# Performance work log

Measured on AMD Instinct MI355X. Metric: run time of the kernel, lower is better.

Reference implementation:

```python
import jax, jax.numpy as jnp
import numpy as np

NUM_FEATURES = 27

def _tril_indices(F):
    idx = []
    for i in range(F):
        for j in range(i):
            idx.append(i * F + j)
    return np.asarray(idx, dtype=np.int32)

TRIL_IDX = _tril_indices(NUM_FEATURES)  # [F*(F-1)/2] = [351]


def setup_inputs() -> dict:
    key = jax.random.key(0)
    k1, k2 = jax.random.split(key)
    B, F, D = 65536, NUM_FEATURES, 128
    features = jax.random.normal(k1, (B, F, D), dtype=jnp.float32)
    bottom_mlp_out = jax.random.normal(k2, (B, D), dtype=jnp.float32)
    return {"features": features, "bottom_mlp_out": bottom_mlp_out}


def reference(features, bottom_mlp_out):
    # features: [B, F, D]
    B = features.shape[0]
    F = features.shape[1]
    # batched Gram matrix: [B, F, F]
    interactions = jnp.einsum('bfd,bgd->bfg', features, features)
    interactions = interactions.reshape(B, F * F)
    # strict lower-triangular pairs: [B, F*(F-1)/2]
    x = interactions[:, TRIL_IDX]
    # concat bottom MLP output in front: [B, D + F*(F-1)/2]
    return jnp.concatenate([bottom_mlp_out, x], axis=1)
```

## Files before the change

### kernel.cpp

```cpp
#include <hip/hip_runtime.h>
#include <stdint.h>

#define NF 27
#define ND 128
#define OUTW 479
#define WAVES 4

typedef float f32x4 __attribute__((ext_vector_type(4)));
typedef short s16x8 __attribute__((ext_vector_type(8)));

__device__ __forceinline__ unsigned short f2bf(float x) {
    union { float f; uint32_t u; } c; c.f = x;
    uint32_t u = c.u;
    u += 0x7fffu + ((u >> 16) & 1u);
    return (unsigned short)(u >> 16);
}

__device__ __forceinline__ s16x8 pack8(float4 a, float4 b) {
    s16x8 r;
    r[0] = (short)f2bf(a.x); r[1] = (short)f2bf(a.y);
    r[2] = (short)f2bf(a.z); r[3] = (short)f2bf(a.w);
    r[4] = (short)f2bf(b.x); r[5] = (short)f2bf(b.y);
    r[6] = (short)f2bf(b.z); r[7] = (short)f2bf(b.w);
    return r;
}

__global__ __launch_bounds__(256) void dot_interact_kernel(
    const float* __restrict__ feat,
    const float* __restrict__ bottom,
    float* __restrict__ out, int B)
{
    const int tid  = threadIdx.x;
    const int lane = tid & 63;
    const int b    = blockIdx.x * WAVES + (tid >> 6);
    if (b >= B) return;

    const int rsel = lane & 15;
    const int kg   = (lane >> 4) * 8;
    const int row1 = (rsel + 16 < NF) ? rsel + 16 : NF - 1;
    const float* fb = feat + (size_t)b * (NF * ND);
    const float* p0 = fb + rsel * ND + kg;
    const float* p1 = fb + row1 * ND + kg;

    f32x4 acc00 = {0.f,0.f,0.f,0.f};
    f32x4 acc10 = {0.f,0.f,0.f,0.f};
    f32x4 acc11 = {0.f,0.f,0.f,0.f};
    #pragma unroll
    for (int ks = 0; ks < 4; ++ks) {
        float4 a0 = *(const float4*)(p0 + ks * 32);
        float4 a1 = *(const float4*)(p0 + ks * 32 + 4);
        float4 b0 = *(const float4*)(p1 + ks * 32);
        float4 b1 = *(const float4*)(p1 + ks * 32 + 4);
        s16x8 fr0 = pack8(a0, a1);
        s16x8 fr1 = pack8(b0, b1);
        acc00 = __builtin_amdgcn_mfma_f32_16x16x32_bf16(fr0, fr0, acc00, 0, 0, 0);
        acc10 = __builtin_amdgcn_mfma_f32_16x16x32_bf16(fr1, fr0, acc10, 0, 0, 0);
        acc11 = __builtin_amdgcn_mfma_f32_16x16x32_bf16(fr1, fr1, acc11, 0, 0, 0);
    }

    float* ob = out + (size_t)b * OUTW;

    const float* bb = bottom + (size_t)b * ND;
    ob[lane]      = bb[lane];
    ob[lane + 64] = bb[lane + 64];

    const int jj = lane & 15;
    const int r0 = (lane >> 4) * 4;
    #pragma unroll
    for (int e = 0; e < 4; ++e) {
        int i0 = r0 + e;
        if (jj < i0) ob[128 + (i0 * (i0 - 1)) / 2 + jj] = acc00[e];
        int i1 = i0 + 16;
        if (i1 < NF) {
            ob[128 + (i1 * (i1 - 1)) / 2 + jj] = acc10[e];
            int j1 = jj + 16;
            if (j1 < i1) ob[128 + (i1 * (i1 - 1)) / 2 + j1] = acc11[e];
        }
    }
}

extern "C" void kernel_launch(void* const* d_in, const int* in_sizes, int n_in,
                              void* d_out, int out_size, void* d_ws, size_t ws_size,
                              hipStream_t stream) {
    const float* feat   = (const float*)d_in[0];
    const float* bottom = (const float*)d_in[1];
    float* out          = (float*)d_out;
    const int B = in_sizes[0] / (NF * ND);
    const int grid = (B + WAVES - 1) / WAVES;
    dot_interact_kernel<<<grid, 256, 0, stream>>>(feat, bottom, out, B);
}
```

Baseline: 205.8 us.

## Stage features through LDS with coalesced loads and double-buffered register prefetch

Each wave now handles four batch rows. It loads the full 27x128 feature tile with coalesced float4 loads into registers, converts it to bf16 and writes it to a padded per-wave LDS region, then reads MFMA fragments from LDS. A second register buffer prefetches the next batch row while the current one is processed, so global loads overlap with compute and stores. The cost is heavy register use (28 float4 per lane), LDS allocation and fewer waves in total, which may lower occupancy. Rows 27-31 of the second MFMA tile read padding in LDS and are never stored.

```diff
diff --git a/kernel.cpp b/kernel.cpp
--- a/kernel.cpp
+++ b/kernel.cpp
@@ -4,7 +4,9 @@
 #define NF 27
 #define ND 128
 #define OUTW 479
+#define LDSROW 136
 #define WAVES 4
+#define NB 4
 
 typedef float f32x4 __attribute__((ext_vector_type(4)));
 typedef short s16x8 __attribute__((ext_vector_type(8)));
@@ -16,66 +18,89 @@
     return (unsigned short)(u >> 16);
 }
 
-__device__ __forceinline__ s16x8 pack8(float4 a, float4 b) {
-    s16x8 r;
-    r[0] = (short)f2bf(a.x); r[1] = (short)f2bf(a.y);
-    r[2] = (short)f2bf(a.z); r[3] = (short)f2bf(a.w);
-    r[4] = (short)f2bf(b.x); r[5] = (short)f2bf(b.y);
-    r[6] = (short)f2bf(b.z); r[7] = (short)f2bf(b.w);
-    return r;
-}
+#define ISSUE(R, B0V, B1V, bidx) do {                                         \
+    long bc_ = (bidx); if (bc_ > (long)B - 1) bc_ = (long)B - 1;              \
+    const float4* f4_ = (const float4*)(feat + bc_ * (NF * ND));              \
+    _Pragma("unroll")                                                         \
+    for (int t_ = 0; t_ < 14; ++t_) {                                         \
+        int fi_ = lane + 64 * t_; if (fi_ > NF * 32 - 1) fi_ = NF * 32 - 1;   \
+        R[t_] = f4_[fi_];                                                     \
+    }                                                                         \
+    const float* bb_ = bottom + bc_ * ND;                                     \
+    B0V = bb_[lane]; B1V = bb_[lane + 64];                                    \
+} while (0)
+
+#define PROCESS(R, B0V, B1V, bidx) do {                                       \
+    if ((bidx) < (long)B) {                                                   \
+        _Pragma("unroll")                                                     \
+        for (int t_ = 0; t_ < 14; ++t_) {                                     \
+            int fi_ = lane + 64 * t_;                                         \
+            if (fi_ < NF * 32) {                                              \
+                int row_ = fi_ >> 5, c4_ = fi_ & 31;                          \
+                uint32_t lo_ = (uint32_t)f2bf(R[t_].x) | ((uint32_t)f2bf(R[t_].y) << 16); \
+                uint32_t hi_ = (uint32_t)f2bf(R[t_].z) | ((uint32_t)f2bf(R[t_].w) << 16); \
+                *(uint2*)(&sm[row_ * LDSROW + c4_ * 4]) = make_uint2(lo_, hi_); \
+            }                                                                 \
+        }                                                                     \
+        asm volatile("s_waitcnt lgkmcnt(0)" ::: "memory");                    \
+        f32x4 acc00 = {0.f,0.f,0.f,0.f};                                      \
+        f32x4 acc10 = {0.f,0.f,0.f,0.f};                                      \
+        f32x4 acc11 = {0.f,0.f,0.f,0.f};                                      \
+        const int rsel_ = lane & 15, ksel_ = (lane >> 4) * 8;                 \
+        _Pragma("unroll")                                                     \
+        for (int ks_ = 0; ks_ < 4; ++ks_) {                                   \
+            int k0_ = ks_ * 32 + ksel_;                                       \
+            s16x8 fr0_ = *(const s16x8*)(&sm[(rsel_     ) * LDSROW + k0_]);   \
+            s16x8 fr1_ = *(const s16x8*)(&sm[(rsel_ + 16) * LDSROW + k0_]);   \
+            acc00 = __builtin_amdgcn_mfma_f32_16x16x32_bf16(fr0_, fr0_, acc00, 0, 0, 0); \
+            acc10 = __builtin_amdgcn_mfma_f32_16x16x32_bf16(fr1_, fr0_, acc10, 0, 0, 0); \
+            acc11 = __builtin_amdgcn_mfma_f32_16x16x32_bf16(fr1_, fr1_, acc11, 0, 0, 0); \
+        }                                                                     \
+        float* ob_ = out + (bidx) * OUTW;                                     \
+        ob_[lane] = B0V; ob_[lane + 64] = B1V;                                \
+        const int jj_ = lane & 15, r0_ = (lane >> 4) * 4;                     \
+        _Pragma("unroll")                                                     \
+        for (int e_ = 0; e_ < 4; ++e_) {                                      \
+            int i0_ = r0_ + e_;                                               \
+            if (jj_ < i0_) ob_[128 + (i0_ * (i0_ - 1)) / 2 + jj_] = acc00[e_];\
+            int i1_ = i0_ + 16;                                               \
+            if (i1_ < NF) {                                                   \
+                ob_[128 + (i1_ * (i1_ - 1)) / 2 + jj_] = acc10[e_];           \
+                int j1_ = jj_ + 16;                                           \
+                if (j1_ < i1_) ob_[128 + (i1_ * (i1_ - 1)) / 2 + j1_] = acc11[e_]; \
+            }                                                                 \
+        }                                                                     \
+        asm volatile("" ::: "memory");  \
+    }                                                                         \
+} while (0)
+
+#define LDS_ALLOC (WAVES * NF * LDSROW + 5 * LDSROW)
 
 __global__ __launch_bounds__(256) void dot_interact_kernel(
     const float* __restrict__ feat,
     const float* __restrict__ bottom,
     float* __restrict__ out, int B)
 {
+    __shared__ unsigned short smem[LDS_ALLOC];
     const int tid  = threadIdx.x;
+    const int w    = tid >> 6;
     const int lane = tid & 63;
-    const int b    = blockIdx.x * WAVES + (tid >> 6);
-    if (b >= B) return;
+    unsigned short* sm = smem + w * (NF * LDSROW);
 
-    const int rsel = lane & 15;
-    const int kg   = (lane >> 4) * 8;
-    const int row1 = (rsel + 16 < NF) ? rsel + 16 : NF - 1;
-    const float* fb = feat + (size_t)b * (NF * ND);
-    const float* p0 = fb + rsel * ND + kg;
-    const float* p1 = fb + row1 * ND + kg;
+    const long wv = (long)blockIdx.x * WAVES + w;
+    const long b0 = wv * NB;
+    if (b0 >= B) return;
 
-    f32x4 acc00 = {0.f,0.f,0.f,0.f};
-    f32x4 acc10 = {0.f,0.f,0.f,0.f};
-    f32x4 acc11 = {0.f,0.f,0.f,0.f};
+    float4 RA[14], RB[14];
+    float a0v, a1v, b0v, b1v;
+
+    ISSUE(RA, a0v, a1v, b0);
     #pragma unroll
-    for (int ks = 0; ks < 4; ++ks) {
-        float4 a0 = *(const float4*)(p0 + ks * 32);
-        float4 a1 = *(const float4*)(p0 + ks * 32 + 4);
-        float4 b0 = *(const float4*)(p1 + ks * 32);
-        float4 b1 = *(const float4*)(p1 + ks * 32 + 4);
-        s16x8 fr0 = pack8(a0, a1);
-        s16x8 fr1 = pack8(b0, b1);
-        acc00 = __builtin_amdgcn_mfma_f32_16x16x32_bf16(fr0, fr0, acc00, 0, 0, 0);
-        acc10 = __builtin_amdgcn_mfma_f32_16x16x32_bf16(fr1, fr0, acc10, 0, 0, 0);
-        acc11 = __builtin_amdgcn_mfma_f32_16x16x32_bf16(fr1, fr1, acc11, 0, 0, 0);
-    }
-
-    float* ob = out + (size_t)b * OUTW;
-
-    const float* bb = bottom + (size_t)b * ND;
-    ob[lane]      = bb[lane];
-    ob[lane + 64] = bb[lane + 64];
-
-    const int jj = lane & 15;
-    const int r0 = (lane >> 4) * 4;
-    #pragma unroll
-    for (int e = 0; e < 4; ++e) {
-        int i0 = r0 + e;
-        if (jj < i0) ob[128 + (i0 * (i0 - 1)) / 2 + jj] = acc00[e];
-        int i1 = i0 + 16;
-        if (i1 < NF) {
-            ob[128 + (i1 * (i1 - 1)) / 2 + jj] = acc10[e];
-            int j1 = jj + 16;
-            if (j1 < i1) ob[128 + (i1 * (i1 - 1)) / 2 + j1] = acc11[e];
-        }
+    for (int i = 0; i < NB; i += 2) {
+        ISSUE(RB, b0v, b1v, b0 + i + 1);
+        PROCESS(RA, a0v, a1v, b0 + i);
+        if (i + 2 < NB) ISSUE(RA, a0v, a1v, b0 + i + 2);
+        PROCESS(RB, b0v, b1v, b0 + i + 1);
     }
 }
 
@@ -86,6 +111,6 @@
     const float* bottom = (const float*)d_in[1];
     float* out          = (float*)d_out;
     const int B = in_sizes[0] / (NF * ND);
-    const int grid = (B + WAVES - 1) / WAVES;
+    const int grid = (B + WAVES * NB - 1) / (WAVES * NB);
     dot_interact_kernel<<<grid, 256, 0, stream>>>(feat, bottom, out, B);
 }
```

Result: slower. 210.0 us (+2.1%).
